# Kernel tuning notes

Measured on AMD Instinct MI355X. Metric: run time of the kernel, lower is better.

The kernel has to match this reference:

```python
import jax, jax.numpy as jnp
import numpy as np

D_MODEL = 1024
N_HEADS = 16
D_FF = 4096
EPS = 1e-5


def setup_inputs() -> dict:
    key = jax.random.key(0)
    ks = jax.random.split(key, 16)
    s = 0.02
    d, f = D_MODEL, D_FF
    return {
        "x": jax.random.normal(ks[0], (4, 2048, d), dtype=jnp.float32),
        "WQ": jax.random.normal(ks[1], (d, d), dtype=jnp.float32) * s,
        "bQ": jnp.zeros((d,), dtype=jnp.float32),
        "WK": jax.random.normal(ks[2], (d, d), dtype=jnp.float32) * s,
        "bK": jnp.zeros((d,), dtype=jnp.float32),
        "WV": jax.random.normal(ks[3], (d, d), dtype=jnp.float32) * s,
        "bV": jnp.zeros((d,), dtype=jnp.float32),
        "WO": jax.random.normal(ks[4], (d, d), dtype=jnp.float32) * s,
        "bO": jnp.zeros((d,), dtype=jnp.float32),
        "W1": jax.random.normal(ks[5], (f, d), dtype=jnp.float32) * s,
        "b1": jnp.zeros((f,), dtype=jnp.float32),
        "W2": jax.random.normal(ks[6], (d, f), dtype=jnp.float32) * s,
        "b2": jnp.zeros((d,), dtype=jnp.float32),
        "g1": jnp.ones((d,), dtype=jnp.float32),
        "be1": jnp.zeros((d,), dtype=jnp.float32),
        "g2": jnp.ones((d,), dtype=jnp.float32),
        "be2": jnp.zeros((d,), dtype=jnp.float32),
    }


def _layernorm(x, g, b):
    mu = jnp.mean(x, axis=-1, keepdims=True)
    var = jnp.mean(jnp.square(x - mu), axis=-1, keepdims=True)
    return (x - mu) * jax.lax.rsqrt(var + EPS) * g + b


def reference(x, WQ, bQ, WK, bK, WV, bV, WO, bO, W1, b1, W2, b2, g1, be1, g2, be2):
    B, T, D = x.shape
    H, dk = N_HEADS, D // N_HEADS
    # projections (torch Linear: x @ W.T + b), reshape to [B,H,T,dk]
    q = (x @ WQ.T + bQ).reshape(B, T, H, dk).transpose(0, 2, 1, 3)
    k = (x @ WK.T + bK).reshape(B, T, H, dk).transpose(0, 2, 1, 3)
    v = (x @ WV.T + bV).reshape(B, T, H, dk).transpose(0, 2, 1, 3)
    scores = jnp.einsum("bhqd,bhkd->bhqk", q, k) / jnp.sqrt(jnp.float32(dk))
    causal = jnp.tril(jnp.ones((T, T), dtype=bool))
    scores = jnp.where(causal[None, None], scores, jnp.float32(-jnp.inf))
    attn = jax.nn.softmax(scores, axis=-1)
    out = jnp.einsum("bhqk,bhkd->bhqd", attn, v)
    out = out.transpose(0, 2, 1, 3).reshape(B, T, D)
    attn_out = out @ WO.T + bO
    x = _layernorm(x + attn_out, g1, be1)
    ff = jax.nn.relu(x @ W1.T + b1) @ W2.T + b2
    return _layernorm(x + ff, g2, be2)
```

## Files before the change

kernel.cpp:

```cpp
#include <hip/hip_runtime.h>

typedef unsigned short u16;
typedef unsigned int u32;
typedef __bf16 bf16x8 __attribute__((ext_vector_type(8)));
typedef float f32x4 __attribute__((ext_vector_type(4)));
typedef float f32x16 __attribute__((ext_vector_type(16)));

__device__ __forceinline__ u16 f2bf(float f) {
  u32 u = __builtin_bit_cast(u32, f);
  u = (u + 0x7fffu + ((u >> 16) & 1u)) >> 16;
  return (u16)u;
}
__device__ __forceinline__ float bf2f(u16 h) {
  return __builtin_bit_cast(float, ((u32)h) << 16);
}

__device__ __forceinline__ void gll16(const u16* g, u16* l) {
  __builtin_amdgcn_global_load_lds((const __attribute__((address_space(1))) void*)g,
                                   (__attribute__((address_space(3))) void*)l, 16, 0, 0);
}

__device__ __forceinline__ void barrier() {
  asm volatile("" ::: "memory");
  __builtin_amdgcn_s_barrier();
  asm volatile("" ::: "memory");
}
__device__ __forceinline__ void waitv3() { asm volatile("s_waitcnt vmcnt(3)" ::: "memory"); }
__device__ __forceinline__ void waitv0() { asm volatile("s_waitcnt vmcnt(0)" ::: "memory"); }

__global__ __launch_bounds__(256) void cvt_all(const float* __restrict__ x,
                                               const float* __restrict__ WQ,
                                               const float* __restrict__ WK,
                                               const float* __restrict__ WV,
                                               const float* __restrict__ WO,
                                               const float* __restrict__ W1,
                                               const float* __restrict__ W2,
                                               u16* __restrict__ xb,
                                               u16* __restrict__ wqkvb,
                                               u16* __restrict__ wob,
                                               u16* __restrict__ w1b,
                                               u16* __restrict__ w2b) {
  const int S = 1 << 20;
  int i = (blockIdx.x * 256 + threadIdx.x) * 4;
  const float* src;
  u16* dst;
  if (i < 8 * S) { src = x + i; dst = xb + i; }
  else {
    int j = i - 8 * S;
    if (j < 3 * S)      { src = (j < S) ? WQ + j : (j < 2 * S) ? WK + (j - S) : WV + (j - 2 * S);
                          dst = wqkvb + j; }
    else if (j < 4 * S) { src = WO + (j - 3 * S); dst = wob + (j - 3 * S); }
    else if (j < 8 * S) { src = W1 + (j - 4 * S); dst = w1b + (j - 4 * S); }
    else                { src = W2 + (j - 8 * S); dst = w2b + (j - 8 * S); }
  }
  float4 v = *(const float4*)src;
  uint2 o;
  o.x = (u32)f2bf(v.x) | ((u32)f2bf(v.y) << 16);
  o.y = (u32)f2bf(v.z) | ((u32)f2bf(v.w) << 16);
  *(uint2*)dst = o;
}

template <int RELU, int QKV, int SPLIT>
__global__ __launch_bounds__(512, 4) void gemm256(const u16* __restrict__ A,
                                                  const u16* __restrict__ W,
                                                  const float* __restrict__ bias0,
                                                  void* __restrict__ C0,
                                                  int M, int N, int K,
                                                  const float* __restrict__ bias1,
                                                  void* __restrict__ C1,
                                                  const float* __restrict__ bias2,
                                                  void* __restrict__ C2,
                                                  int NBN) {
  __shared__ alignas(16) u16 lds[2 * 12288];
  const int tid = threadIdx.x;
  const int id = blockIdx.x;
  const int xcd = id & 7, r = id >> 3;
  int bm, bn, kz = 0, koff = 0, KL = K;
  if (SPLIT) {
    bn = (r & 7) << 7;
    const int q = r >> 3;
    bm = ((q & 3) * 8 + xcd) << 8;
    kz = q >> 2;
    KL = K >> 1;
    koff = kz * KL;
  } else {
    bn = (r % NBN) << 7;
    bm = ((r / NBN) * 8 + xcd) << 8;
  }
  const int wave = tid >> 6, lane = tid & 63;
  const int lr = lane & 15, quad = lane >> 4;
  const int wm = (wave >> 1) << 6;
  const int wn = (wave & 1) << 6;

  const int lrow = lane >> 2;
  const int lch = (lane & 3) ^ ((lane >> 3) & 3);
  const u16* Asrc = A + (size_t)(bm + wave * 32 + lrow) * K + koff + lch * 8;
  const u16* Wsrc = W + (size_t)(bn + wave * 16 + lrow) * K + koff + lch * 8;
  const size_t rK16 = (size_t)16 * K;

  const int NT = KL >> 5;
  const int fro = (quad ^ ((lr >> 1) & 3)) * 8;
  f32x4 acc[4][4] = {};

#define STAGE(tt) { const int tp_ = ((tt) < NT) ? (tt) : NT - 1;    \
    const size_t ko_ = (size_t)tp_ * 32;                                                            \
    u16* b_ = lds + ((tt) & 1) * 12288;                                                             \
    gll16(Asrc + ko_, b_ + wave * 1024);                                                            \
    gll16(Asrc + ko_ + rK16, b_ + wave * 1024 + 512);                                               \
    gll16(Wsrc + ko_, b_ + 8192 + wave * 512); }

  STAGE(0);

  for (int t = 0; t < NT; t++) {
    barrier();
    STAGE(t + 1);
    waitv3();
    barrier();
    const u16* sa = lds + (t & 1) * 12288;
    const u16* sb = sa + 8192;
    bf16x8 af[4], bfr[4];
    #pragma unroll
    for (int mi = 0; mi < 4; mi++)
      af[mi] = *(const bf16x8*)(sa + (wm + mi * 16 + lr) * 32 + fro);
    #pragma unroll
    for (int ni = 0; ni < 4; ni++)
      bfr[ni] = *(const bf16x8*)(sb + (wn + ni * 16 + lr) * 32 + fro);
    asm volatile("s_waitcnt lgkmcnt(0)" ::: "memory");
    __builtin_amdgcn_s_setprio(1);
    #pragma unroll
    for (int mi = 0; mi < 4; mi++)
      #pragma unroll
      for (int ni = 0; ni < 4; ni++)
        acc[mi][ni] = __builtin_amdgcn_mfma_f32_16x16x32_bf16(af[mi], bfr[ni], acc[mi][ni], 0, 0, 0);
    __builtin_amdgcn_s_setprio(0);
  }
  waitv0();
#undef STAGE

  const float* bp = bias0;
  void* outp = C0;
  float scale = 1.0f;
  int cb = bn, Nout = N, seg = 0;
  if (QKV) {
    Nout = 1024;
    seg = bn >> 10;
    cb = bn & 1023;
    if (seg == 0) scale = 0.125f * 1.44269504089f;
    else if (seg == 1) { bp = bias1; outp = C1; }
    else { bp = bias2; outp = C2; }
  }
  if (SPLIT && kz) outp = C1;

  if (QKV && seg == 2) {
    #pragma unroll
    for (int ni = 0; ni < 4; ni++) {
      const int col = cb + wn + ni * 16 + lr;
      const int hh = col >> 6, dl = col & 63;
      const float bv = bp[col];
      #pragma unroll
      for (int mi = 0; mi < 4; mi++) {
        const int row0 = bm + wm + mi * 16 + quad * 4;
        const int bb = row0 >> 11, tt = row0 & 2047;
        u16 pk[4];
        #pragma unroll
        for (int rg = 0; rg < 4; rg++) pk[rg] = f2bf(acc[mi][ni][rg] + bv);
        uint2 val;
        val.x = (u32)pk[0] | ((u32)pk[1] << 16);
        val.y = (u32)pk[2] | ((u32)pk[3] << 16);
        *(uint2*)(((u16*)outp) + ((size_t)((bb * 16 + hh) * 64 + dl)) * 2048 + tt) = val;
      }
    }
    return;
  }

  #pragma unroll
  for (int ni = 0; ni < 4; ni++) {
    const int col = cb + wn + ni * 16 + lr;
    const float bv = (SPLIT && kz) ? 0.0f : bp[col];
    #pragma unroll
    for (int mi = 0; mi < 4; mi++) {
      #pragma unroll
      for (int rg = 0; rg < 4; rg++) {
        int row = bm + wm + mi * 16 + quad * 4 + rg;
        float v = (acc[mi][ni][rg] + bv) * scale;
        if (RELU) v = fmaxf(v, 0.0f);
        ((u16*)outp)[(size_t)row * Nout + col] = f2bf(v);
      }
    }
  }
}

__global__ __launch_bounds__(256) void attn_mfma(const u16* __restrict__ qb,
                                                 const u16* __restrict__ kb,
                                                 const u16* __restrict__ vt,
                                                 u16* __restrict__ ctxb, int T) {
  __shared__ alignas(16) u16 shm[4 * 4096];
  const int tid = threadIdx.x;
  const int i = blockIdx.x;
  const int g = i & 63;
  const int p = 31 - (i >> 6);
  const int h = g >> 2, b = g & 3;
  const size_t base = ((size_t)(b * T)) * 1024 + h * 64;
  const size_t vbase = ((size_t)((b * 16 + h) * 64)) * T;
  const int lane = tid & 63, wave = tid >> 6;
  const int l31 = lane & 31, hh = lane >> 5;
  const int sub = wave & 1;
  const int kh = wave >> 1;
  const int srow = lane >> 3;
  const int sch = ((lane & 7) ^ srow) * 8;
  const int fs8 = l31 & 7;
  const int q0w = p * 64 + sub * 32;

  bf16x8 qf[4];
  #pragma unroll
  for (int ds = 0; ds < 4; ds++) {
    uint4 uq = *(const uint4*)(qb + base + (size_t)(q0w + l31) * 1024 + ds * 16 + hh * 8);
    qf[ds] = __builtin_bit_cast(bf16x8, uq);
  }
  f32x16 o0 = {}, o1 = {};
  float rsum = 0.0f;

  const int NI = (p >> 1) + 1;
  for (int j = 0; j < NI; j++) {
    const int ke = 2 * j;
    const int ko = (2 * j + 1 <= p) ? 2 * j + 1 : p;
    barrier();
    #pragma unroll
    for (int jj = 0; jj < 2; jj++) {
      const int rb = wave * 16 + jj * 8;
      const int rr = rb + srow;
      gll16(kb + base + (size_t)(ke * 64 + rr) * 1024 + sch, shm + rb * 64);
      gll16(kb + base + (size_t)(ko * 64 + rr) * 1024 + sch, shm + 4096 + rb * 64);
      gll16(vt + vbase + (size_t)rr * T + (size_t)(ke * 64) + sch, shm + 8192 + rb * 64);
      gll16(vt + vbase + (size_t)rr * T + (size_t)(ko * 64) + sch, shm + 12288 + rb * 64);
    }
    waitv0();
    barrier();
    const int kt = 2 * j + kh;
    if (kt <= p) {
      const u16* sKc = shm + kh * 4096;
      const u16* sVc = shm + 8192 + kh * 4096;

      f32x16 s0v = {}, s1v = {};
      #pragma unroll
      for (int ds = 0; ds < 4; ds++) {
        const int co = ((2 * ds + hh) ^ fs8) * 8;
        bf16x8 kf0 = *(const bf16x8*)(sKc + l31 * 64 + co);
        bf16x8 kf1 = *(const bf16x8*)(sKc + (32 + l31) * 64 + co);
        s0v = __builtin_amdgcn_mfma_f32_32x32x16_bf16(kf0, qf[ds], s0v, 0, 0, 0);
        s1v = __builtin_amdgcn_mfma_f32_32x32x16_bf16(kf1, qf[ds], s1v, 0, 0, 0);
      }

      if (kt == p) {
        const int qloc = (sub << 5) + l31;
        #pragma unroll
        for (int rg = 0; rg < 16; rg++) {
          const int key = (rg & 3) + 8 * (rg >> 2) + 4 * hh;
          if (key > qloc) s0v[rg] = -1e30f;
          if (key + 32 > qloc) s1v[rg] = -1e30f;
        }
      }

      float e[32];
      #pragma unroll
      for (int rg = 0; rg < 16; rg++) {
        e[rg] = __builtin_amdgcn_exp2f(s0v[rg]);
        e[16 + rg] = __builtin_amdgcn_exp2f(s1v[rg]);
        rsum += e[rg] + e[16 + rg];
      }

      union PW { u32 w[4]; bf16x8 v; } pf[4];
      #pragma unroll
      for (int t = 0; t < 2; t++) {
        #pragma unroll
        for (int sl = 0; sl < 2; sl++) {
          const int rb = t * 16 + sl * 8;
          u32 wa = __builtin_amdgcn_perm(__builtin_bit_cast(u32, e[rb + 1]), __builtin_bit_cast(u32, e[rb + 0]), 0x07060302u);
          u32 wb = __builtin_amdgcn_perm(__builtin_bit_cast(u32, e[rb + 5]), __builtin_bit_cast(u32, e[rb + 4]), 0x07060302u);
          u32 wc = __builtin_amdgcn_perm(__builtin_bit_cast(u32, e[rb + 3]), __builtin_bit_cast(u32, e[rb + 2]), 0x07060302u);
          u32 wd = __builtin_amdgcn_perm(__builtin_bit_cast(u32, e[rb + 7]), __builtin_bit_cast(u32, e[rb + 6]), 0x07060302u);
          asm("v_permlane32_swap_b32 %0, %1" : "+v"(wa), "+v"(wb));
          asm("v_permlane32_swap_b32 %0, %1" : "+v"(wc), "+v"(wd));
          pf[t * 2 + sl].w[0] = wa; pf[t * 2 + sl].w[1] = wc;
          pf[t * 2 + sl].w[2] = wb; pf[t * 2 + sl].w[3] = wd;
        }
      }

      #pragma unroll
      for (int s = 0; s < 4; s++) {
        const int co = ((2 * s + hh) ^ fs8) * 8;
        bf16x8 vf0 = *(const bf16x8*)(sVc + l31 * 64 + co);
        bf16x8 vf1 = *(const bf16x8*)(sVc + (32 + l31) * 64 + co);
        o0 = __builtin_amdgcn_mfma_f32_32x32x16_bf16(pf[s].v, vf0, o0, 0, 0, 0);
        o1 = __builtin_amdgcn_mfma_f32_32x32x16_bf16(pf[s].v, vf1, o1, 0, 0, 0);
      }
    }
  }

  rsum += __shfl_xor(rsum, 32);
  barrier();
  float* red = (float*)shm;
  if (kh == 1) {
    #pragma unroll
    for (int rg = 0; rg < 16; rg++) {
      red[sub * 2112 + rg * 64 + lane] = o0[rg];
      red[sub * 2112 + (16 + rg) * 64 + lane] = o1[rg];
    }
    red[sub * 2112 + 2048 + lane] = rsum;
  }
  barrier();
  if (kh == 0) {
    #pragma unroll
    for (int rg = 0; rg < 16; rg++) {
      o0[rg] += red[sub * 2112 + rg * 64 + lane];
      o1[rg] += red[sub * 2112 + (16 + rg) * 64 + lane];
    }
    rsum += red[sub * 2112 + 2048 + lane];
    float inv = 1.0f / rsum;
    #pragma unroll
    for (int rg = 0; rg < 16; rg++) {
      const int qr = (rg & 3) + 8 * (rg >> 2) + 4 * hh;
      float iv = __shfl(inv, qr);
      const size_t rowoff = base + (size_t)(q0w + qr) * 1024;
      ctxb[rowoff + l31] = f2bf(o0[rg] * iv);
      ctxb[rowoff + 32 + l31] = f2bf(o1[rg] * iv);
    }
  }
}

template <int ABF>
__global__ __launch_bounds__(256) void ln_kernel(const void* __restrict__ a,
                                                 const u16* __restrict__ b,
                                                 const u16* __restrict__ c,
                                                 const float* __restrict__ g,
                                                 const float* __restrict__ be,
                                                 float* __restrict__ of32,
                                                 u16* __restrict__ obf) {
  const int row = blockIdx.x;
  const int tid = threadIdx.x;
  const size_t base = (size_t)row * 1024;
  const int cc = tid * 4;
  float a0, a1, a2, a3;
  if (ABF) {
    uint2 ua = *(const uint2*)((const u16*)a + base + cc);
    a0 = bf2f(ua.x & 0xffff); a1 = bf2f(ua.x >> 16);
    a2 = bf2f(ua.y & 0xffff); a3 = bf2f(ua.y >> 16);
  } else {
    float4 xa = *(const float4*)((const float*)a + base + cc);
    a0 = xa.x; a1 = xa.y; a2 = xa.z; a3 = xa.w;
  }
  uint2 ub = *(const uint2*)(b + base + cc);
  uint2 uc = *(const uint2*)(c + base + cc);
  float v0 = a0 + bf2f(ub.x & 0xffff) + bf2f(uc.x & 0xffff);
  float v1 = a1 + bf2f(ub.x >> 16)    + bf2f(uc.x >> 16);
  float v2 = a2 + bf2f(ub.y & 0xffff) + bf2f(uc.y & 0xffff);
  float v3 = a3 + bf2f(ub.y >> 16)    + bf2f(uc.y >> 16);
  float s1 = v0 + v1 + v2 + v3;
  float s2 = v0 * v0 + v1 * v1 + v2 * v2 + v3 * v3;
  for (int off = 1; off < 64; off <<= 1) {
    s1 += __shfl_xor(s1, off);
    s2 += __shfl_xor(s2, off);
  }
  __shared__ float red[8];
  int wv = tid >> 6;
  if ((tid & 63) == 0) { red[wv] = s1; red[4 + wv] = s2; }
  __syncthreads();
  s1 = red[0] + red[1] + red[2] + red[3];
  s2 = red[4] + red[5] + red[6] + red[7];
  float mu = s1 * (1.0f / 1024.0f);
  float var = s2 * (1.0f / 1024.0f) - mu * mu;
  float rs = rsqrtf(var + 1e-5f);
  float4 gv = *(const float4*)(g + cc);
  float4 bev = *(const float4*)(be + cc);
  float y0 = (v0 - mu) * rs * gv.x + bev.x;
  float y1 = (v1 - mu) * rs * gv.y + bev.y;
  float y2 = (v2 - mu) * rs * gv.z + bev.z;
  float y3 = (v3 - mu) * rs * gv.w + bev.w;
  if (of32) {
    float4 o = make_float4(y0, y1, y2, y3);
    *(float4*)(of32 + base + cc) = o;
  }
  if (obf) {
    uint2 o;
    o.x = (u32)f2bf(y0) | ((u32)f2bf(y1) << 16);
    o.y = (u32)f2bf(y2) | ((u32)f2bf(y3) << 16);
    *(uint2*)(obf + base + cc) = o;
  }
}

extern "C" void kernel_launch(void* const* d_in, const int* in_sizes, int n_in,
                              void* d_out, int out_size, void* d_ws, size_t ws_size,
                              hipStream_t stream) {
  const int Mtok = 8192, D = 1024, F = 4096, T = 2048;
  const float* x   = (const float*)d_in[0];
  const float* WQ  = (const float*)d_in[1];
  const float* bQ  = (const float*)d_in[2];
  const float* WK  = (const float*)d_in[3];
  const float* bK  = (const float*)d_in[4];
  const float* WV  = (const float*)d_in[5];
  const float* bV  = (const float*)d_in[6];
  const float* WO  = (const float*)d_in[7];
  const float* bO  = (const float*)d_in[8];
  const float* W1  = (const float*)d_in[9];
  const float* b1  = (const float*)d_in[10];
  const float* W2  = (const float*)d_in[11];
  const float* b2  = (const float*)d_in[12];
  const float* g1  = (const float*)d_in[13];
  const float* be1 = (const float*)d_in[14];
  const float* g2  = (const float*)d_in[15];
  const float* be2 = (const float*)d_in[16];

  char* ws = (char*)d_ws;
  const size_t MB = 1024 * 1024;
  u16*  xb     = (u16*)(ws + 0);
  u16*  wqkvb  = (u16*)(ws + 16 * MB);
  u16*  wob    = (u16*)(ws + 22 * MB);
  u16*  w1b    = (u16*)(ws + 24 * MB);
  u16*  w2b    = (u16*)(ws + 32 * MB);
  u16*  qb     = (u16*)(ws + 40 * MB);
  u16*  kb     = (u16*)(ws + 56 * MB);
  u16*  vtb    = (u16*)(ws + 72 * MB);
  u16*  ctxb   = (u16*)(ws + 88 * MB);
  u16*  wp0    = (u16*)(ws + 104 * MB);
  u16*  wp1    = (u16*)(ws + 120 * MB);
  u16*  h1b    = (u16*)(ws + 136 * MB);
  u16*  ff1b   = (u16*)(ws + 40 * MB);
  u16*  fp0    = (u16*)(ws + 0);
  u16*  fp1    = (u16*)(ws + 16 * MB);
  float* out   = (float*)d_out;

  dim3 blk(256);
  dim3 blk512(512);
  cvt_all<<<(20 << 20) / 1024, blk, 0, stream>>>(x, WQ, WK, WV, WO, W1, W2,
                                                 xb, wqkvb, wob, w1b, w2b);

  gemm256<0, 1, 0><<<dim3(768), blk512, 0, stream>>>(xb, wqkvb, bQ, qb, Mtok, 3072, D,
                                                     bK, kb, bV, vtb, 24);
  attn_mfma<<<dim3(2048), blk, 0, stream>>>(qb, kb, vtb, ctxb, T);

  gemm256<0, 0, 1><<<dim3(512), blk512, 0, stream>>>(ctxb, wob, bO, wp0, Mtok, D, D,
                                                     nullptr, wp1, nullptr, nullptr, 8);
  ln_kernel<0><<<Mtok, blk, 0, stream>>>(x, wp0, wp1, g1, be1, nullptr, h1b);

  gemm256<1, 0, 0><<<dim3(1024), blk512, 0, stream>>>(h1b, w1b, b1, ff1b, Mtok, F, D,
                                                      nullptr, nullptr, nullptr, nullptr, 32);
  gemm256<0, 0, 1><<<dim3(512), blk512, 0, stream>>>(ff1b, w2b, b2, fp0, Mtok, D, F,
                                                     nullptr, fp1, nullptr, nullptr, 8);
  ln_kernel<1><<<Mtok, blk, 0, stream>>>(h1b, fp0, fp1, g2, be2, out, (u16*)nullptr);
}
```

Baseline: 455.1 us.

## Restructure attention blocks to 128 queries with double-buffered K/V prefetch

The attention kernel now gives each workgroup 128 queries, one 32-row slice per wave, in place of 64 queries with the key range split across wave pairs. This removes the shared-memory cross-wave reduction and halves the grid. K/V tiles are staged one tile ahead into a two-slot LDS buffer with a partial vmcnt wait, so loads overlap compute. In exchange, parallelism per block is lower, there are fewer workgroups, and waves in the same block sit idle at different causal boundaries.

After: 457.2 us. About the same (+0.4%).

```diff
diff --git a/kernel.cpp b/kernel.cpp
--- a/kernel.cpp
+++ b/kernel.cpp
@@ -25,6 +25,7 @@
   __builtin_amdgcn_s_barrier();
   asm volatile("" ::: "memory");
 }
+__device__ __forceinline__ void waitv4() { asm volatile("s_waitcnt vmcnt(4)" ::: "memory"); }
 __device__ __forceinline__ void waitv3() { asm volatile("s_waitcnt vmcnt(3)" ::: "memory"); }
 __device__ __forceinline__ void waitv0() { asm volatile("s_waitcnt vmcnt(0)" ::: "memory"); }
 
@@ -194,22 +195,30 @@
                                                  const u16* __restrict__ kb,
                                                  const u16* __restrict__ vt,
                                                  u16* __restrict__ ctxb, int T) {
-  __shared__ alignas(16) u16 shm[4 * 4096];
+  __shared__ alignas(16) u16 shm[2][8192];
   const int tid = threadIdx.x;
   const int i = blockIdx.x;
   const int g = i & 63;
-  const int p = 31 - (i >> 6);
+  const int qb0 = 15 - (i >> 6);
   const int h = g >> 2, b = g & 3;
   const size_t base = ((size_t)(b * T)) * 1024 + h * 64;
   const size_t vbase = ((size_t)((b * 16 + h) * 64)) * T;
   const int lane = tid & 63, wave = tid >> 6;
   const int l31 = lane & 31, hh = lane >> 5;
-  const int sub = wave & 1;
-  const int kh = wave >> 1;
   const int srow = lane >> 3;
   const int sch = ((lane & 7) ^ srow) * 8;
   const int fs8 = l31 & 7;
-  const int q0w = p * 64 + sub * 32;
+  const int q0w = qb0 * 128 + wave * 32;
+  const int NK = 2 * qb0 + 2;
+
+#define STAGEKV(ktt, slot) {                                                        \
+    const int kc_ = ((ktt) < NK) ? (ktt) : NK - 1;                                  \
+    _Pragma("unroll") for (int j_ = 0; j_ < 2; j_++) {                              \
+      const int rb_ = wave * 16 + j_ * 8;                                           \
+      const int rr_ = rb_ + srow;                                                   \
+      gll16(kb + base + (size_t)(kc_ * 64 + rr_) * 1024 + sch, shm[slot] + rb_ * 64);\
+      gll16(vt + vbase + (size_t)rr_ * T + (size_t)(kc_ * 64) + sch, shm[slot] + 4096 + rb_ * 64);\
+    } }
 
   bf16x8 qf[4];
   #pragma unroll
@@ -220,26 +229,17 @@
   f32x16 o0 = {}, o1 = {};
   float rsum = 0.0f;
 
-  const int NI = (p >> 1) + 1;
-  for (int j = 0; j < NI; j++) {
-    const int ke = 2 * j;
-    const int ko = (2 * j + 1 <= p) ? 2 * j + 1 : p;
+  STAGEKV(0, 0);
+
+  for (int kt = 0; kt < NK; kt++) {
     barrier();
-    #pragma unroll
-    for (int jj = 0; jj < 2; jj++) {
-      const int rb = wave * 16 + jj * 8;
-      const int rr = rb + srow;
-      gll16(kb + base + (size_t)(ke * 64 + rr) * 1024 + sch, shm + rb * 64);
-      gll16(kb + base + (size_t)(ko * 64 + rr) * 1024 + sch, shm + 4096 + rb * 64);
-      gll16(vt + vbase + (size_t)rr * T + (size_t)(ke * 64) + sch, shm + 8192 + rb * 64);
-      gll16(vt + vbase + (size_t)rr * T + (size_t)(ko * 64) + sch, shm + 12288 + rb * 64);
-    }
-    waitv0();
+    STAGEKV(kt + 1, (kt + 1) & 1);
+    waitv4();
     barrier();
-    const int kt = 2 * j + kh;
-    if (kt <= p) {
-      const u16* sKc = shm + kh * 4096;
-      const u16* sVc = shm + 8192 + kh * 4096;
+    const int kq = kt * 64;
+    if (kq <= q0w + 31) {
+      const u16* sKc = shm[kt & 1];
+      const u16* sVc = shm[kt & 1] + 4096;
 
       f32x16 s0v = {}, s1v = {};
       #pragma unroll
@@ -251,13 +251,13 @@
         s1v = __builtin_amdgcn_mfma_f32_32x32x16_bf16(kf1, qf[ds], s1v, 0, 0, 0);
       }
 
-      if (kt == p) {
-        const int qloc = (sub << 5) + l31;
+      if (kq + 63 > q0w) {
+        const int qg = q0w + l31;
         #pragma unroll
         for (int rg = 0; rg < 16; rg++) {
-          const int key = (rg & 3) + 8 * (rg >> 2) + 4 * hh;
-          if (key > qloc) s0v[rg] = -1e30f;
-          if (key + 32 > qloc) s1v[rg] = -1e30f;
+          const int key = kq + (rg & 3) + 8 * (rg >> 2) + 4 * hh;
+          if (key > qg) s0v[rg] = -1e30f;
+          if (key + 32 > qg) s1v[rg] = -1e30f;
         }
       }
 
@@ -296,35 +296,18 @@
       }
     }
   }
+  waitv0();
+#undef STAGEKV
 
   rsum += __shfl_xor(rsum, 32);
-  barrier();
-  float* red = (float*)shm;
-  if (kh == 1) {
-    #pragma unroll
-    for (int rg = 0; rg < 16; rg++) {
-      red[sub * 2112 + rg * 64 + lane] = o0[rg];
-      red[sub * 2112 + (16 + rg) * 64 + lane] = o1[rg];
-    }
-    red[sub * 2112 + 2048 + lane] = rsum;
-  }
-  barrier();
-  if (kh == 0) {
-    #pragma unroll
-    for (int rg = 0; rg < 16; rg++) {
-      o0[rg] += red[sub * 2112 + rg * 64 + lane];
-      o1[rg] += red[sub * 2112 + (16 + rg) * 64 + lane];
-    }
-    rsum += red[sub * 2112 + 2048 + lane];
-    float inv = 1.0f / rsum;
-    #pragma unroll
-    for (int rg = 0; rg < 16; rg++) {
-      const int qr = (rg & 3) + 8 * (rg >> 2) + 4 * hh;
-      float iv = __shfl(inv, qr);
-      const size_t rowoff = base + (size_t)(q0w + qr) * 1024;
-      ctxb[rowoff + l31] = f2bf(o0[rg] * iv);
-      ctxb[rowoff + 32 + l31] = f2bf(o1[rg] * iv);
-    }
+  float inv = 1.0f / rsum;
+  #pragma unroll
+  for (int rg = 0; rg < 16; rg++) {
+    const int qr = (rg & 3) + 8 * (rg >> 2) + 4 * hh;
+    float iv = __shfl(inv, qr);
+    const size_t rowoff = base + (size_t)(q0w + qr) * 1024;
+    ctxb[rowoff + l31] = f2bf(o0[rg] * iv);
+    ctxb[rowoff + 32 + l31] = f2bf(o1[rg] * iv);
   }
 }
 
@@ -436,7 +419,7 @@
 
   gemm256<0, 1, 0><<<dim3(768), blk512, 0, stream>>>(xb, wqkvb, bQ, qb, Mtok, 3072, D,
                                                      bK, kb, bV, vtb, 24);
-  attn_mfma<<<dim3(2048), blk, 0, stream>>>(qb, kb, vtb, ctxb, T);
+  attn_mfma<<<dim3(1024), blk, 0, stream>>>(qb, kb, vtb, ctxb, T);
 
   gemm256<0, 0, 1><<<dim3(512), blk512, 0, stream>>>(ctxb, wob, bO, wp0, Mtok, D, D,
                                                      nullptr, wp1, nullptr, nullptr, 8);
```
